# Kernel tuning notes

Hardware: AMD Instinct MI355X
Metric: run time of the kernel (lower is better)

The kernel has to match this reference:

```python
import jax, jax.numpy as jnp
import numpy as np

B, C, NH = 8, 256, 8
HD = C // NH
SCALE = HD ** -0.5
SHAPES = [(56, 56), (28, 28)]          # (H,W) per branch
SRS = [8, 4]                            # conv kernel=stride per branch
EPS = 1e-5


def layer_norm(x, w, b):
    mu = x.mean(-1, keepdims=True)
    var = ((x - mu) ** 2).mean(-1, keepdims=True)
    return (x - mu) * jax.lax.rsqrt(var + EPS) * w + b


def setup_inputs() -> dict:
    key = jax.random.key(0)
    ks = jax.random.split(key, 8)
    std = 0.02
    inp = {
        'x0': jax.random.normal(ks[0], (B, 3136, C), jnp.float32),
        'x1': jax.random.normal(ks[1], (B, 784, C), jnp.float32),
        'q_w': jax.random.normal(ks[2], (C, C), jnp.float32) * std,
        'kv_w': jax.random.normal(ks[3], (2 * C, C), jnp.float32) * std,
        'proj_w': jax.random.normal(ks[4], (C, C), jnp.float32) * std,
        'proj_b': jnp.zeros((C,), jnp.float32),
        'sr0_w': jax.random.normal(ks[5], (C, C, 8, 8), jnp.float32) * np.sqrt(2.0 / (8 * 8 * C)),
        'sr0_b': jnp.zeros((C,), jnp.float32),
        'sr1_w': jax.random.normal(ks[6], (C, C, 4, 4), jnp.float32) * np.sqrt(2.0 / (4 * 4 * C)),
        'sr1_b': jnp.zeros((C,), jnp.float32),
        'norm0_w': jnp.ones((C,), jnp.float32),
        'norm0_b': jnp.zeros((C,), jnp.float32),
        'norm1_w': jnp.ones((C,), jnp.float32),
        'norm1_b': jnp.zeros((C,), jnp.float32),
    }
    return inp


def reference(x0, x1, q_w, kv_w, proj_w, proj_b, sr0_w, sr0_b, sr1_w, sr1_b,
              norm0_w, norm0_b, norm1_w, norm1_b):
    xs = [x0, x1]
    sr_ws = [sr0_w, sr1_w]
    sr_bs = [sr0_b, sr1_b]
    norm_ws = [norm0_w, norm1_w]
    norm_bs = [norm0_b, norm1_b]

    Qs, Ks, Vs = [], [], []
    for x, (H, W), s, sw, sb, nw, nb in zip(xs, SHAPES, SRS, sr_ws, sr_bs, norm_ws, norm_bs):
        N = H * W
        # q projection -> [B, NH, N, HD]
        q = (x @ q_w.T).reshape(B, N, NH, HD).transpose(0, 2, 1, 3)
        Qs.append(q)
        # spatial reduction: [B,N,C] -> [B,C,H,W] -> strided conv -> [B, N', C]
        xi = x.transpose(0, 2, 1).reshape(B, C, H, W)
        xr = jax.lax.conv_general_dilated(
            xi, sw, window_strides=(s, s), padding='VALID',
            dimension_numbers=('NCHW', 'OIHW', 'NCHW')) + sb[None, :, None, None]
        Np = (H // s) * (W // s)
        xr = xr.reshape(B, C, Np).transpose(0, 2, 1)
        xr = layer_norm(xr, nw, nb)
        kv = (xr @ kv_w.T).reshape(B, Np, 2, NH, HD).transpose(2, 0, 3, 1, 4)
        Ks.append(kv[0])
        Vs.append(kv[1])

    Q = jnp.concatenate(Qs, axis=2)   # [B, NH, Nq, HD]
    K = jnp.concatenate(Ks, axis=2)   # [B, NH, Nk, HD]
    V = jnp.concatenate(Vs, axis=2)

    attn = jnp.einsum('bhqd,bhkd->bhqk', Q, K) * SCALE
    attn = jax.nn.softmax(attn, axis=-1)
    X = jnp.einsum('bhqk,bhkd->bhqd', attn, V)
    X = X.transpose(0, 2, 1, 3).reshape(B, -1, C)
    return X @ proj_w.T + proj_b
```

## Files before the change

### kernel.cpp

```cpp
#include <hip/hip_runtime.h>

typedef unsigned short u16;
typedef unsigned int u32;
typedef float f4 __attribute__((ext_vector_type(4)));
typedef short s8v __attribute__((ext_vector_type(8)));
typedef unsigned short u16x4 __attribute__((ext_vector_type(4)));

__device__ __forceinline__ u16 f2bf(float f) {
    u32 u = __float_as_uint(f);
    u32 r = (u + 0x7FFFu + ((u >> 16) & 1u)) >> 16;
    return (u16)r;
}

#define GLDS16(g, l)                                                                   \
    __builtin_amdgcn_global_load_lds((const __attribute__((address_space(1))) u32*)(g),\
                                     (__attribute__((address_space(3))) u32*)(l), 16, 0, 0)

__global__ __launch_bounds__(256) void prep_kernel(
    const float* __restrict__ x0, const float* __restrict__ x1,
    const float* __restrict__ qw, const float* __restrict__ kvw,
    const float* __restrict__ pw, const float* __restrict__ w0,
    const float* __restrict__ w1,
    u16* __restrict__ x0b, u16* __restrict__ x1b, u16* __restrict__ qwb,
    u16* __restrict__ kvwb, u16* __restrict__ pwb,
    u16* __restrict__ Wc0, u16* __restrict__ Wc1)
{
    for (int u = blockIdx.x * 256 + threadIdx.x; u < 3383296; u += gridDim.x * 256) {
        if (u < 2072576) {
            const float* src; u16* dst; int idx;
            if (u < 1605632)      { src = x0;  dst = x0b;  idx = u; }
            else if (u < 2007040) { src = x1;  dst = x1b;  idx = u - 1605632; }
            else if (u < 2023424) { src = qw;  dst = qwb;  idx = u - 2007040; }
            else if (u < 2056192) { src = kvw; dst = kvwb; idx = u - 2023424; }
            else                  { src = pw;  dst = pwb;  idx = u - 2056192; }
            f4 v = *(const f4*)(src + (size_t)idx * 4);
            u16x4 o;
            o[0] = f2bf(v[0]); o[1] = f2bf(v[1]); o[2] = f2bf(v[2]); o[3] = f2bf(v[3]);
            *(u16x4*)(dst + (size_t)idx * 4) = o;
        } else if (u < 3121152) {
            int e = (u - 2072576) * 4;
            int o = e >> 14, rem = e & 16383;
            int khw = rem >> 8, c = rem & 255;
            u16x4 ov;
            #pragma unroll
            for (int j = 0; j < 4; ++j)
                ov[j] = f2bf(w0[(size_t)o * 16384 + (size_t)(c + j) * 64 + khw]);
            *(u16x4*)(Wc0 + (size_t)e) = ov;
        } else {
            int e = (u - 3121152) * 4;
            int o = e >> 12, rem = e & 4095;
            int khw = rem >> 8, c = rem & 255;
            u16x4 ov;
            #pragma unroll
            for (int j = 0; j < 4; ++j)
                ov[j] = f2bf(w1[(size_t)o * 4096 + (size_t)(c + j) * 16 + khw]);
            *(u16x4*)(Wc1 + (size_t)e) = ov;
        }
    }
}

__global__ __launch_bounds__(256) void qc_kernel(
    const u16* __restrict__ x0b, const u16* __restrict__ x1b,
    const u16* __restrict__ qwb, u16* __restrict__ Yq,
    const u16* __restrict__ Wc0, const u16* __restrict__ Wc1,
    float* __restrict__ xr0, float* __restrict__ xr1)
{
    __shared__ u16 lsA[128 * 64];
    __shared__ u16 lsB[128 * 64];
    int bid = blockIdx.x;
    int tid = threadIdx.x;
    int w = tid >> 6, l = tid & 63, g = l >> 4, lq = l & 15;
    int wr = w >> 1, wc = w & 1;

    f4 acc[4][4];
    #pragma unroll
    for (int i = 0; i < 4; ++i)
        #pragma unroll
        for (int j = 0; j < 4; ++j) acc[i][j] = (f4){0.f, 0.f, 0.f, 0.f};

    if (bid < 496) {
        int x = bid & 1, y = (bid >> 1) % 31, bz = bid / 62;
        int m0 = y * 128, n0 = x * 128;
        const u16* aptr[4];
        long boff[4];
        #pragma unroll
        for (int i = 0; i < 4; ++i) {
            int p = (w * 4 + i) * 64 + l;
            int r = p >> 3, cp = p & 7;
            int ar = m0 + r; ar = ar < 3920 ? ar : 3919;
            const u16* base = (ar < 3136)
                ? x0b + ((size_t)bz * 3136 + ar) * 256
                : x1b + ((size_t)bz * 784 + (ar - 3136)) * 256;
            aptr[i] = base + ((cp ^ (r & 7)) << 3);
            boff[i] = (long)(n0 + r) * 256 + ((cp ^ (r & 7)) << 3);
        }
        for (int k0 = 0; k0 < 256; k0 += 64) {
            __syncthreads();
            #pragma unroll
            for (int i = 0; i < 4; ++i)
                GLDS16(aptr[i] + k0, &lsA[(w * 4 + i) * 512]);
            #pragma unroll
            for (int i = 0; i < 4; ++i)
                GLDS16(qwb + boff[i] + k0, &lsB[(w * 4 + i) * 512]);
            __syncthreads();
            #pragma unroll
            for (int kk = 0; kk < 2; ++kk) {
                s8v af[4], bf[4];
                #pragma unroll
                for (int mf = 0; mf < 4; ++mf) {
                    int row = wr * 64 + mf * 16 + lq;
                    int ph = (kk * 4 + g) ^ (row & 7);
                    af[mf] = *(const s8v*)&lsA[row * 64 + ph * 8];
                }
                #pragma unroll
                for (int nf = 0; nf < 4; ++nf) {
                    int row = wc * 64 + nf * 16 + lq;
                    int ph = (kk * 4 + g) ^ (row & 7);
                    bf[nf] = *(const s8v*)&lsB[row * 64 + ph * 8];
                }
                #pragma unroll
                for (int mf = 0; mf < 4; ++mf)
                    #pragma unroll
                    for (int nf = 0; nf < 4; ++nf)
                        acc[mf][nf] = __builtin_amdgcn_mfma_f32_16x16x32_bf16(
                            af[mf], bf[nf], acc[mf][nf], 0, 0, 0);
            }
        }
        #pragma unroll
        for (int mf = 0; mf < 4; ++mf)
            #pragma unroll
            for (int r = 0; r < 4; ++r) {
                int grow = m0 + wr * 64 + mf * 16 + g * 4 + r;
                if (grow < 3920) {
                    #pragma unroll
                    for (int nf = 0; nf < 4; ++nf) {
                        int col = n0 + wc * 64 + nf * 16 + lq;
                        Yq[((size_t)bz * 3920 + grow) * 256 + col] = f2bf(acc[mf][nf][r]);
                    }
                }
            }
    } else {
        int cb = bid - 496;
        int bx = cb & 1, by = (cb >> 1) & 3, z = cb >> 3;
        const u16* Xb; const u16* Wcp; float* Co;
        int Npix, Wimg, lgs, Kc, zz;
        if (z < 16) { Xb = x0b; Wcp = Wc0; Co = xr0; Npix = 3136; Wimg = 56; lgs = 3; Kc = 16384; zz = z; }
        else        { Xb = x1b; Wcp = Wc1; Co = xr1; Npix = 784;  Wimg = 28; lgs = 2; Kc = 4096;  zz = z - 16; }
        int s = 1 << lgs;
        int m0 = by * 128, n0 = bx * 128;

        long aoff[4], boff[4];
        #pragma unroll
        for (int i = 0; i < 4; ++i) {
            int p = (w * 4 + i) * 64 + l;
            int r = p >> 3, cp = p & 7;
            int rr = m0 + r; rr = rr < 392 ? rr : 391;
            int bb = rr / 49, pp = rr % 49;
            int ph = pp / 7, pw = pp % 7;
            aoff[i] = ((long)bb * Npix + (long)(ph * Wimg + pw) * s) * 256 + ((cp ^ (r & 7)) << 3);
            boff[i] = (long)(n0 + r) * Kc + ((cp ^ (r & 7)) << 3);
        }
        int kbase = zz * 1024;
        for (int ko = 0; ko < 1024; ko += 64) {
            int k0 = kbase + ko;
            int khw = k0 >> 8;
            int kh = khw >> lgs, kw = khw & (s - 1);
            long adelta = (long)(kh * Wimg + kw) * 256 + (k0 & 255);
            __syncthreads();
            #pragma unroll
            for (int i = 0; i < 4; ++i)
                GLDS16(Xb + aoff[i] + adelta, &lsA[(w * 4 + i) * 512]);
            #pragma unroll
            for (int i = 0; i < 4; ++i)
                GLDS16(Wcp + boff[i] + k0, &lsB[(w * 4 + i) * 512]);
            __syncthreads();
            #pragma unroll
            for (int kk = 0; kk < 2; ++kk) {
                s8v af[4], bf[4];
                #pragma unroll
                for (int mf = 0; mf < 4; ++mf) {
                    int row = wr * 64 + mf * 16 + lq;
                    int ph2 = (kk * 4 + g) ^ (row & 7);
                    af[mf] = *(const s8v*)&lsA[row * 64 + ph2 * 8];
                }
                #pragma unroll
                for (int nf = 0; nf < 4; ++nf) {
                    int row = wc * 64 + nf * 16 + lq;
                    int ph2 = (kk * 4 + g) ^ (row & 7);
                    bf[nf] = *(const s8v*)&lsB[row * 64 + ph2 * 8];
                }
                #pragma unroll
                for (int mf = 0; mf < 4; ++mf)
                    #pragma unroll
                    for (int nf = 0; nf < 4; ++nf)
                        acc[mf][nf] = __builtin_amdgcn_mfma_f32_16x16x32_bf16(
                            af[mf], bf[nf], acc[mf][nf], 0, 0, 0);
            }
        }
        float* Cb = Co + (size_t)zz * 392 * 256;
        #pragma unroll
        for (int mf = 0; mf < 4; ++mf)
            #pragma unroll
            for (int r = 0; r < 4; ++r) {
                int grow = m0 + wr * 64 + mf * 16 + g * 4 + r;
                if (grow < 392) {
                    #pragma unroll
                    for (int nf = 0; nf < 4; ++nf) {
                        int col = n0 + wc * 64 + nf * 16 + lq;
                        Cb[(size_t)grow * 256 + col] = acc[mf][nf][r];
                    }
                }
            }
    }
}

__global__ __launch_bounds__(256) void ln_kernel(
    const float* __restrict__ xr0, const float* __restrict__ xr1,
    const float* __restrict__ srb0, const float* __restrict__ srb1,
    const float* __restrict__ n0w, const float* __restrict__ n0b,
    const float* __restrict__ n1w, const float* __restrict__ n1b,
    u16* __restrict__ lnb)
{
    int row = blockIdx.x;
    int b = row / 98, j = row % 98;
    int c = threadIdx.x;
    const float* src; int sidx, ns;
    const float *bs, *nw, *nb;
    if (j < 49) { src = xr0; sidx = b * 49 + j;       ns = 16; bs = srb0; nw = n0w; nb = n0b; }
    else        { src = xr1; sidx = b * 49 + (j - 49); ns = 4; bs = srb1; nw = n1w; nb = n1b; }
    float v = bs[c];
    for (int sl = 0; sl < ns; ++sl) v += src[(size_t)sl * 100352 + (size_t)sidx * 256 + c];
    __shared__ float red[8];
    float sumv = v;
    #pragma unroll
    for (int off = 32; off; off >>= 1) sumv += __shfl_down(sumv, off, 64);
    int wid = c >> 6, lane = c & 63;
    if (lane == 0) red[wid] = sumv;
    __syncthreads();
    float mu = (red[0] + red[1] + red[2] + red[3]) * (1.0f / 256.0f);
    float dv = v - mu;
    float s2 = dv * dv;
    #pragma unroll
    for (int off = 32; off; off >>= 1) s2 += __shfl_down(s2, off, 64);
    if (lane == 0) red[4 + wid] = s2;
    __syncthreads();
    float var = (red[4] + red[5] + red[6] + red[7]) * (1.0f / 256.0f);
    float rr = rsqrtf(var + 1e-5f);
    lnb[(size_t)row * 256 + c] = f2bf(dv * rr * nw[c] + nb[c]);
}

__global__ __launch_bounds__(256) void kv_kernel(
    const u16* __restrict__ A, const u16* __restrict__ Bw,
    u16* __restrict__ Kb, u16* __restrict__ Vtb)
{
    __shared__ u16 lsA[128 * 64];
    __shared__ u16 lsB[128 * 64];
    int tid = threadIdx.x;
    int w = tid >> 6, l = tid & 63, g = l >> 4, lq = l & 15;
    int wr = w >> 1, wc = w & 1;
    int n0 = blockIdx.x * 128;
    int bz = blockIdx.z;
    const u16* Ab = A + (size_t)bz * 98 * 256;

    long aoff[4], boff[4];
    #pragma unroll
    for (int i = 0; i < 4; ++i) {
        int p = (w * 4 + i) * 64 + l;
        int r = p >> 3, cp = p & 7;
        int ar = r < 98 ? r : 97;
        aoff[i] = (long)ar * 256 + ((cp ^ (r & 7)) << 3);
        boff[i] = (long)(n0 + r) * 256 + ((cp ^ (r & 7)) << 3);
    }
    f4 acc[4][4];
    #pragma unroll
    for (int i = 0; i < 4; ++i)
        #pragma unroll
        for (int j = 0; j < 4; ++j) acc[i][j] = (f4){0.f, 0.f, 0.f, 0.f};

    for (int k0 = 0; k0 < 256; k0 += 64) {
        __syncthreads();
        #pragma unroll
        for (int i = 0; i < 4; ++i)
            GLDS16(Ab + aoff[i] + k0, &lsA[(w * 4 + i) * 512]);
        #pragma unroll
        for (int i = 0; i < 4; ++i)
            GLDS16(Bw + boff[i] + k0, &lsB[(w * 4 + i) * 512]);
        __syncthreads();
        #pragma unroll
        for (int kk = 0; kk < 2; ++kk) {
            s8v af[4], bf[4];
            #pragma unroll
            for (int mf = 0; mf < 4; ++mf) {
                int row = wr * 64 + mf * 16 + lq;
                int ph = (kk * 4 + g) ^ (row & 7);
                af[mf] = *(const s8v*)&lsA[row * 64 + ph * 8];
            }
            #pragma unroll
            for (int nf = 0; nf < 4; ++nf) {
                int row = wc * 64 + nf * 16 + lq;
                int ph = (kk * 4 + g) ^ (row & 7);
                bf[nf] = *(const s8v*)&lsB[row * 64 + ph * 8];
            }
            #pragma unroll
            for (int mf = 0; mf < 4; ++mf)
                #pragma unroll
                for (int nf = 0; nf < 4; ++nf)
                    acc[mf][nf] = __builtin_amdgcn_mfma_f32_16x16x32_bf16(
                        af[mf], bf[nf], acc[mf][nf], 0, 0, 0);
        }
    }
    #pragma unroll
    for (int mf = 0; mf < 4; ++mf)
        #pragma unroll
        for (int r = 0; r < 4; ++r) {
            int grow = wr * 64 + mf * 16 + g * 4 + r;
            #pragma unroll
            for (int nf = 0; nf < 4; ++nf) {
                int col = n0 + wc * 64 + nf * 16 + lq;
                u16 bv = (grow < 98) ? f2bf(acc[mf][nf][r]) : (u16)0;
                if (col < 256) {
                    if (grow < 112)
                        Kb[((size_t)(bz * 8 + (col >> 5)) * 112 + grow) * 32 + (col & 31)] = bv;
                } else {
                    int cc = col - 256;
                    Vtb[((size_t)(bz * 8 + (cc >> 5)) * 32 + (cc & 31)) * 128 + grow] = bv;
                }
            }
        }
}

#define SCALE_F 0.1767766952966369f
__global__ __launch_bounds__(512) void attnout_kernel(
    const u16* __restrict__ Yq, const u16* __restrict__ Kb,
    const u16* __restrict__ Vtb, const u16* __restrict__ pwb,
    const float* __restrict__ proj_b, float* __restrict__ out)
{
    __shared__ u16 Ps[8][16 * 128];
    __shared__ u16 Os[64 * 256];
    int tid = threadIdx.x;
    int w = tid >> 6, l = tid & 63, g = l >> 4, lq = l & 15;
    int b = blockIdx.y, h = w;
    int n0 = blockIdx.x * 64;
    const u16* Kh = Kb + (size_t)(b * 8 + h) * 112 * 32;
    const u16* Vh = Vtb + (size_t)(b * 8 + h) * 32 * 128;
    u16* Pw = Ps[w];

    if (l < 32) {
        int row = l >> 1;
        int gr = (14 + (l & 1)) ^ (row & 7);
        *(s8v*)&Pw[row * 128 + gr * 8] = (s8v){0, 0, 0, 0, 0, 0, 0, 0};
    }

    for (int qt = 0; qt < 4; ++qt) {
        int qrow = n0 + qt * 16 + lq;
        int qr = qrow < 3920 ? qrow : 3919;
        s8v qf = *(const s8v*)(Yq + ((size_t)b * 3920 + qr) * 256 + h * 32 + g * 8);
        f4 sacc[7];
        #pragma unroll
        for (int f = 0; f < 7; ++f) {
            s8v kf = *(const s8v*)(Kh + (f * 16 + lq) * 32 + g * 8);
            f4 zz = (f4){0.f, 0.f, 0.f, 0.f};
            sacc[f] = __builtin_amdgcn_mfma_f32_16x16x32_bf16(kf, qf, zz, 0, 0, 0);
        }
        float pm = -1e30f;
        float sv[7][4];
        #pragma unroll
        for (int f = 0; f < 7; ++f)
            #pragma unroll
            for (int r = 0; r < 4; ++r) {
                int key = f * 16 + g * 4 + r;
                float v = sacc[f][r] * SCALE_F;
                if (key >= 98) v = -1e30f;
                sv[f][r] = v;
                pm = fmaxf(pm, v);
            }
        pm = fmaxf(pm, __shfl_xor(pm, 16));
        pm = fmaxf(pm, __shfl_xor(pm, 32));
        float sum = 0.f;
        float pv[7][4];
        #pragma unroll
        for (int f = 0; f < 7; ++f)
            #pragma unroll
            for (int r = 0; r < 4; ++r) {
                float e = __expf(sv[f][r] - pm);
                pv[f][r] = e;
                sum += e;
            }
        sum += __shfl_xor(sum, 16);
        sum += __shfl_xor(sum, 32);
        float inv = 1.0f / sum;

        #pragma unroll
        for (int f = 0; f < 7; ++f)
            #pragma unroll
            for (int pr = 0; pr < 2; ++pr) {
                u32 pk = (u32)f2bf(pv[f][2 * pr] * inv) |
                         ((u32)f2bf(pv[f][2 * pr + 1] * inv) << 16);
                int k = f * 16 + g * 4 + pr * 2;
                int gr = (k >> 3) ^ (lq & 7);
                *(u32*)&Pw[lq * 128 + gr * 8 + (k & 7)] = pk;
            }

        f4 o0 = (f4){0.f, 0.f, 0.f, 0.f}, o1 = (f4){0.f, 0.f, 0.f, 0.f};
        #pragma unroll
        for (int s4 = 0; s4 < 4; ++s4) {
            int gv = s4 * 4 + g;
            s8v pa = *(const s8v*)&Pw[lq * 128 + ((gv ^ (lq & 7)) * 8)];
            s8v vf0 = *(const s8v*)(Vh + (size_t)lq * 128 + s4 * 32 + g * 8);
            s8v vf1 = *(const s8v*)(Vh + (size_t)(16 + lq) * 128 + s4 * 32 + g * 8);
            o0 = __builtin_amdgcn_mfma_f32_16x16x32_bf16(pa, vf0, o0, 0, 0, 0);
            o1 = __builtin_amdgcn_mfma_f32_16x16x32_bf16(pa, vf1, o1, 0, 0, 0);
        }
        #pragma unroll
        for (int r = 0; r < 4; ++r) {
            int R = qt * 16 + g * 4 + r;
            #pragma unroll
            for (int half = 0; half < 2; ++half) {
                int C = h * 32 + half * 16 + lq;
                int sg = (C >> 3) ^ (R & 7);
                Os[R * 256 + sg * 8 + (C & 7)] = f2bf(half ? o1[r] : o0[r]);
            }
        }
    }
    __syncthreads();

    f4 acc[4][2];
    #pragma unroll
    for (int i = 0; i < 4; ++i) {
        acc[i][0] = (f4){0.f, 0.f, 0.f, 0.f};
        acc[i][1] = (f4){0.f, 0.f, 0.f, 0.f};
    }
    for (int k0 = 0; k0 < 256; k0 += 32) {
        s8v af[4], bf[2];
        int kgr = (k0 >> 3) + g;
        #pragma unroll
        for (int mf = 0; mf < 4; ++mf) {
            int row = mf * 16 + lq;
            af[mf] = *(const s8v*)&Os[row * 256 + ((kgr ^ (row & 7)) * 8)];
        }
        #pragma unroll
        for (int nf = 0; nf < 2; ++nf) {
            int n = w * 32 + nf * 16 + lq;
            bf[nf] = *(const s8v*)(pwb + (size_t)n * 256 + k0 + g * 8);
        }
        #pragma unroll
        for (int mf = 0; mf < 4; ++mf)
            #pragma unroll
            for (int nf = 0; nf < 2; ++nf)
                acc[mf][nf] = __builtin_amdgcn_mfma_f32_16x16x32_bf16(
                    af[mf], bf[nf], acc[mf][nf], 0, 0, 0);
    }
    #pragma unroll
    for (int mf = 0; mf < 4; ++mf)
        #pragma unroll
        for (int r = 0; r < 4; ++r) {
            int grow = n0 + mf * 16 + g * 4 + r;
            if (grow < 3920) {
                #pragma unroll
                for (int nf = 0; nf < 2; ++nf) {
                    int col = w * 32 + nf * 16 + lq;
                    out[((size_t)b * 3920 + grow) * 256 + col] = acc[mf][nf][r] + proj_b[col];
                }
            }
        }
}

extern "C" void kernel_launch(void* const* d_in, const int* in_sizes, int n_in,
                              void* d_out, int out_size, void* d_ws, size_t ws_size,
                              hipStream_t stream)
{
    const float* x0     = (const float*)d_in[0];
    const float* x1     = (const float*)d_in[1];
    const float* q_w    = (const float*)d_in[2];
    const float* kv_w   = (const float*)d_in[3];
    const float* proj_w = (const float*)d_in[4];
    const float* proj_b = (const float*)d_in[5];
    const float* sr0_w  = (const float*)d_in[6];
    const float* sr0_b  = (const float*)d_in[7];
    const float* sr1_w  = (const float*)d_in[8];
    const float* sr1_b  = (const float*)d_in[9];
    const float* n0w    = (const float*)d_in[10];
    const float* n0b    = (const float*)d_in[11];
    const float* n1w    = (const float*)d_in[12];
    const float* n1b    = (const float*)d_in[13];
    (void)in_sizes; (void)n_in; (void)out_size; (void)ws_size;

    float* ws = (float*)d_ws;
    u16*  Yq   = (u16*)ws;
    u16*  x0b  = (u16*)(ws + 4014080);
    u16*  x1b  = (u16*)(ws + 7225344);
    float* xr0 = ws + 8028160;
    float* xr1 = ws + 9633792;
    u16*  Kb   = (u16*)(ws + 10035200);
    u16*  Vtb  = (u16*)(ws + 10149888);
    u16*  qwb  = (u16*)(ws + 10280960);
    u16*  kvwb = (u16*)(ws + 10313728);
    u16*  pwb  = (u16*)(ws + 10379264);
    u16*  Wc0  = (u16*)(ws + 10412032);
    u16*  Wc1  = (u16*)(ws + 12509184);
    u16*  lnb  = (u16*)(ws + 13033472);

    prep_kernel<<<2048, 256, 0, stream>>>(
        x0, x1, q_w, kv_w, proj_w, sr0_w, sr1_w,
        x0b, x1b, qwb, kvwb, pwb, Wc0, Wc1);

    qc_kernel<<<656, 256, 0, stream>>>(x0b, x1b, qwb, Yq, Wc0, Wc1, xr0, xr1);

    ln_kernel<<<784, 256, 0, stream>>>(xr0, xr1, sr0_b, sr1_b, n0w, n0b, n1w, n1b, lnb);

    kv_kernel<<<dim3(4, 1, 8), 256, 0, stream>>>(lnb, kvwb, Kb, Vtb);

    attnout_kernel<<<dim3(62, 8), 512, 0, stream>>>(
        Yq, Kb, Vtb, pwb, proj_b, (float*)d_out);
}
```

Measured before the change: 108.6 us.

## Double-buffer LDS tiles in GEMM kernels to overlap global loads with MFMA

The q-projection/conv GEMM kernel and the kv GEMM kernel now use two LDS buffers per operand. The next K-tile is prefetched with global_load_lds while MFMAs run on the current tile, so each iteration needs one barrier instead of two. This doubles LDS use per block to 64KB, which can lower occupancy. Correctness depends on the barrier at the end of each iteration also covering completion of the async LDS loads.

```diff
diff --git a/kernel.cpp b/kernel.cpp
--- a/kernel.cpp
+++ b/kernel.cpp
@@ -65,8 +65,8 @@
     const u16* __restrict__ Wc0, const u16* __restrict__ Wc1,
     float* __restrict__ xr0, float* __restrict__ xr1)
 {
-    __shared__ u16 lsA[128 * 64];
-    __shared__ u16 lsB[128 * 64];
+    __shared__ u16 lsA[2][128 * 64];
+    __shared__ u16 lsB[2][128 * 64];
     int bid = blockIdx.x;
     int tid = threadIdx.x;
     int w = tid >> 6, l = tid & 63, g = l >> 4, lq = l & 15;
@@ -94,15 +94,26 @@
             aptr[i] = base + ((cp ^ (r & 7)) << 3);
             boff[i] = (long)(n0 + r) * 256 + ((cp ^ (r & 7)) << 3);
         }
-        for (int k0 = 0; k0 < 256; k0 += 64) {
-            __syncthreads();
-            #pragma unroll
-            for (int i = 0; i < 4; ++i)
-                GLDS16(aptr[i] + k0, &lsA[(w * 4 + i) * 512]);
-            #pragma unroll
-            for (int i = 0; i < 4; ++i)
-                GLDS16(qwb + boff[i] + k0, &lsB[(w * 4 + i) * 512]);
-            __syncthreads();
+        #pragma unroll
+        for (int i = 0; i < 4; ++i)
+            GLDS16(aptr[i], &lsA[0][(w * 4 + i) * 512]);
+        #pragma unroll
+        for (int i = 0; i < 4; ++i)
+            GLDS16(qwb + boff[i], &lsB[0][(w * 4 + i) * 512]);
+        __syncthreads();
+        int cur = 0;
+        for (int t = 0; t < 4; ++t) {
+            if (t < 3) {
+                int kn = (t + 1) * 64;
+                #pragma unroll
+                for (int i = 0; i < 4; ++i)
+                    GLDS16(aptr[i] + kn, &lsA[cur ^ 1][(w * 4 + i) * 512]);
+                #pragma unroll
+                for (int i = 0; i < 4; ++i)
+                    GLDS16(qwb + boff[i] + kn, &lsB[cur ^ 1][(w * 4 + i) * 512]);
+            }
+            const u16* pA = lsA[cur];
+            const u16* pB = lsB[cur];
             #pragma unroll
             for (int kk = 0; kk < 2; ++kk) {
                 s8v af[4], bf[4];
@@ -110,13 +121,13 @@
                 for (int mf = 0; mf < 4; ++mf) {
                     int row = wr * 64 + mf * 16 + lq;
                     int ph = (kk * 4 + g) ^ (row & 7);
-                    af[mf] = *(const s8v*)&lsA[row * 64 + ph * 8];
+                    af[mf] = *(const s8v*)&pA[row * 64 + ph * 8];
                 }
                 #pragma unroll
                 for (int nf = 0; nf < 4; ++nf) {
                     int row = wc * 64 + nf * 16 + lq;
                     int ph = (kk * 4 + g) ^ (row & 7);
-                    bf[nf] = *(const s8v*)&lsB[row * 64 + ph * 8];
+                    bf[nf] = *(const s8v*)&pB[row * 64 + ph * 8];
                 }
                 #pragma unroll
                 for (int mf = 0; mf < 4; ++mf)
@@ -125,6 +136,8 @@
                         acc[mf][nf] = __builtin_amdgcn_mfma_f32_16x16x32_bf16(
                             af[mf], bf[nf], acc[mf][nf], 0, 0, 0);
             }
+            __syncthreads();
+            cur ^= 1;
         }
         #pragma unroll
         for (int mf = 0; mf < 4; ++mf)
@@ -161,19 +174,35 @@
             boff[i] = (long)(n0 + r) * Kc + ((cp ^ (r & 7)) << 3);
         }
         int kbase = zz * 1024;
-        for (int ko = 0; ko < 1024; ko += 64) {
-            int k0 = kbase + ko;
+        {
+            int k0 = kbase;
             int khw = k0 >> 8;
             int kh = khw >> lgs, kw = khw & (s - 1);
             long adelta = (long)(kh * Wimg + kw) * 256 + (k0 & 255);
-            __syncthreads();
             #pragma unroll
             for (int i = 0; i < 4; ++i)
-                GLDS16(Xb + aoff[i] + adelta, &lsA[(w * 4 + i) * 512]);
+                GLDS16(Xb + aoff[i] + adelta, &lsA[0][(w * 4 + i) * 512]);
             #pragma unroll
             for (int i = 0; i < 4; ++i)
-                GLDS16(Wcp + boff[i] + k0, &lsB[(w * 4 + i) * 512]);
-            __syncthreads();
+                GLDS16(Wcp + boff[i] + k0, &lsB[0][(w * 4 + i) * 512]);
+        }
+        __syncthreads();
+        int cur = 0;
+        for (int t = 0; t < 16; ++t) {
+            if (t < 15) {
+                int k0 = kbase + (t + 1) * 64;
+                int khw = k0 >> 8;
+                int kh = khw >> lgs, kw = khw & (s - 1);
+                long adelta = (long)(kh * Wimg + kw) * 256 + (k0 & 255);
+                #pragma unroll
+                for (int i = 0; i < 4; ++i)
+                    GLDS16(Xb + aoff[i] + adelta, &lsA[cur ^ 1][(w * 4 + i) * 512]);
+                #pragma unroll
+                for (int i = 0; i < 4; ++i)
+                    GLDS16(Wcp + boff[i] + k0, &lsB[cur ^ 1][(w * 4 + i) * 512]);
+            }
+            const u16* pA = lsA[cur];
+            const u16* pB = lsB[cur];
             #pragma unroll
             for (int kk = 0; kk < 2; ++kk) {
                 s8v af[4], bf[4];
@@ -181,13 +210,13 @@
                 for (int mf = 0; mf < 4; ++mf) {
                     int row = wr * 64 + mf * 16 + lq;
                     int ph2 = (kk * 4 + g) ^ (row & 7);
-                    af[mf] = *(const s8v*)&lsA[row * 64 + ph2 * 8];
+                    af[mf] = *(const s8v*)&pA[row * 64 + ph2 * 8];
                 }
                 #pragma unroll
                 for (int nf = 0; nf < 4; ++nf) {
                     int row = wc * 64 + nf * 16 + lq;
                     int ph2 = (kk * 4 + g) ^ (row & 7);
-                    bf[nf] = *(const s8v*)&lsB[row * 64 + ph2 * 8];
+                    bf[nf] = *(const s8v*)&pB[row * 64 + ph2 * 8];
                 }
                 #pragma unroll
                 for (int mf = 0; mf < 4; ++mf)
@@ -196,6 +225,8 @@
                         acc[mf][nf] = __builtin_amdgcn_mfma_f32_16x16x32_bf16(
                             af[mf], bf[nf], acc[mf][nf], 0, 0, 0);
             }
+            __syncthreads();
+            cur ^= 1;
         }
         float* Cb = Co + (size_t)zz * 392 * 256;
         #pragma unroll
@@ -253,8 +284,8 @@
     const u16* __restrict__ A, const u16* __restrict__ Bw,
     u16* __restrict__ Kb, u16* __restrict__ Vtb)
 {
-    __shared__ u16 lsA[128 * 64];
-    __shared__ u16 lsB[128 * 64];
+    __shared__ u16 lsA[2][128 * 64];
+    __shared__ u16 lsB[2][128 * 64];
     int tid = threadIdx.x;
     int w = tid >> 6, l = tid & 63, g = l >> 4, lq = l & 15;
     int wr = w >> 1, wc = w & 1;
@@ -277,15 +308,26 @@
         #pragma unroll
         for (int j = 0; j < 4; ++j) acc[i][j] = (f4){0.f, 0.f, 0.f, 0.f};
 
-    for (int k0 = 0; k0 < 256; k0 += 64) {
-        __syncthreads();
-        #pragma unroll
-        for (int i = 0; i < 4; ++i)
-            GLDS16(Ab + aoff[i] + k0, &lsA[(w * 4 + i) * 512]);
-        #pragma unroll
-        for (int i = 0; i < 4; ++i)
-            GLDS16(Bw + boff[i] + k0, &lsB[(w * 4 + i) * 512]);
-        __syncthreads();
+    #pragma unroll
+    for (int i = 0; i < 4; ++i)
+        GLDS16(Ab + aoff[i], &lsA[0][(w * 4 + i) * 512]);
+    #pragma unroll
+    for (int i = 0; i < 4; ++i)
+        GLDS16(Bw + boff[i], &lsB[0][(w * 4 + i) * 512]);
+    __syncthreads();
+    int cur = 0;
+    for (int t = 0; t < 4; ++t) {
+        if (t < 3) {
+            int kn = (t + 1) * 64;
+            #pragma unroll
+            for (int i = 0; i < 4; ++i)
+                GLDS16(Ab + aoff[i] + kn, &lsA[cur ^ 1][(w * 4 + i) * 512]);
+            #pragma unroll
+            for (int i = 0; i < 4; ++i)
+                GLDS16(Bw + boff[i] + kn, &lsB[cur ^ 1][(w * 4 + i) * 512]);
+        }
+        const u16* pA = lsA[cur];
+        const u16* pB = lsB[cur];
         #pragma unroll
         for (int kk = 0; kk < 2; ++kk) {
             s8v af[4], bf[4];
@@ -293,13 +335,13 @@
             for (int mf = 0; mf < 4; ++mf) {
                 int row = wr * 64 + mf * 16 + lq;
                 int ph = (kk * 4 + g) ^ (row & 7);
-                af[mf] = *(const s8v*)&lsA[row * 64 + ph * 8];
+                af[mf] = *(const s8v*)&pA[row * 64 + ph * 8];
             }
             #pragma unroll
             for (int nf = 0; nf < 4; ++nf) {
                 int row = wc * 64 + nf * 16 + lq;
                 int ph = (kk * 4 + g) ^ (row & 7);
-                bf[nf] = *(const s8v*)&lsB[row * 64 + ph * 8];
+                bf[nf] = *(const s8v*)&pB[row * 64 + ph * 8];
             }
             #pragma unroll
             for (int mf = 0; mf < 4; ++mf)
@@ -308,6 +350,8 @@
                     acc[mf][nf] = __builtin_amdgcn_mfma_f32_16x16x32_bf16(
                         af[mf], bf[nf], acc[mf][nf], 0, 0, 0);
         }
+        __syncthreads();
+        cur ^= 1;
     }
     #pragma unroll
     for (int mf = 0; mf < 4; ++mf)
```

Measured after the change: 114.2 us. 5.1% more time.
